# Optimization experiments

Measured on AMD Instinct MI355X. Metric: run time of the kernel, lower is better.

The kernel has to match this reference:

```python
import jax, jax.numpy as jnp
import numpy as np

H = 100  # hidden size

def setup_inputs() -> dict:
    key = jax.random.key(0)
    ks = jax.random.split(key, 7)
    B, T = 512, 1024
    s = 1.0 / np.sqrt(H)  # pytorch LSTMCell/Linear init scale
    return {
        "input": jax.random.normal(ks[0], (B, T), dtype=jnp.float32),
        "W_ih": jax.random.uniform(ks[1], (4 * H, 1), jnp.float32, -s, s),
        "W_hh": jax.random.uniform(ks[2], (4 * H, H), jnp.float32, -s, s),
        "b_ih": jax.random.uniform(ks[3], (4 * H,), jnp.float32, -s, s),
        "b_hh": jax.random.uniform(ks[4], (4 * H,), jnp.float32, -s, s),
        "W_out": jax.random.uniform(ks[5], (1, H), jnp.float32, -s, s),
        "b_out": jax.random.uniform(ks[6], (1,), jnp.float32, -s, s),
    }

def reference(input, W_ih, W_hh, b_ih, b_hh, W_out, b_out):
    B, T = input.shape
    dt = input.dtype
    # Precompute the input projection for all steps at once: [T, B, 4H]
    # (input_size == 1, so this is an outer product with W_ih[:, 0])
    x_proj = input.T[:, :, None] * W_ih[:, 0][None, None, :] + (b_ih + b_hh)

    def step(carry, xp_t):
        h, c = carry
        gates = xp_t + h @ W_hh.T  # [B, 4H]
        i, f, g, o = jnp.split(gates, 4, axis=1)  # PyTorch gate order i,f,g,o
        i = jax.nn.sigmoid(i)
        f = jax.nn.sigmoid(f)
        g = jnp.tanh(g)
        o = jax.nn.sigmoid(o)
        c_new = f * c + i * g
        h_new = o * jnp.tanh(c_new)
        out_t = h_new @ W_out.T + b_out  # [B, 1]
        return (h_new, c_new), out_t[:, 0]

    h0 = jnp.zeros((B, H), dtype=dt)
    c0 = jnp.zeros((B, H), dtype=dt)
    _, outs = jax.lax.scan(step, (h0, c0), x_proj)  # outs: [T, B]
    return outs.T  # [B, T]
```

## Files before the change

kernel.cpp:

```cpp
#include <hip/hip_runtime.h>


#define HID   100
#define TLEN  1024
#define NB    8
#define BLOCK 896
#define INSTR 1033
#define SC_LO 0.00048828125f
#define SC_HI 2048.0f

typedef _Float16 half8 __attribute__((ext_vector_type(8)));
typedef float    f32x4 __attribute__((ext_vector_type(4)));

#define MFMA(A,B,C) __builtin_amdgcn_mfma_f32_16x16x32_f16((A),(B),(C),0,0,0)
#define LOG2E   1.442695041f
#define LOG2E2  2.885390082f
#define RCP(x)  __builtin_amdgcn_rcpf(x)

static __device__ __forceinline__ unsigned packh(_Float16 a, _Float16 b) {
    return (unsigned)__builtin_bit_cast(unsigned short, a)
         | ((unsigned)__builtin_bit_cast(unsigned short, b) << 16);
}
static __device__ __forceinline__ float exp2v(float x) {
    float r;
    asm("v_exp_f32 %0, %1" : "=v"(r) : "v"(x));
    return r;
}

__global__ __launch_bounds__(BLOCK, 1)
void lstm_mfma5(
    const float* __restrict__ input,
    const float* __restrict__ W_ih,
    const float* __restrict__ W_hh,
    const float* __restrict__ b_ih,
    const float* __restrict__ b_hh,
    const float* __restrict__ W_out,
    const float* __restrict__ b_out,
    float* __restrict__ out)
{
    const int tid  = threadIdx.x;
    const int lane = tid & 63;
    const int w    = tid >> 6;
    const int b0   = blockIdx.x * NB;
    const int q    = lane >> 4;
    const int col  = lane & 15;
    const int side = (col >> 3) & 1;
    const int bat  = lane & 7;

    __shared__ __align__(16) unsigned B_lds[2][4][64][4];
    __shared__ float in_s[NB * INSTR];

    for (int i = tid; i < NB * TLEN; i += BLOCK) {
        const int n = i >> 10, t = i & 1023;
        in_s[n * INSTR + t] = input[(b0 + n) * TLEN + t];
    }
    for (int i = tid; i < 2 * 4 * 64 * 4; i += BLOCK)
        ((unsigned*)B_lds)[i] = 0u;

    const int nt = (w < 12) ? 2 : ((w == 12) ? 1 : 0);
    const int tb = 2 * w;

    half8 A[2][4];
    if (w < 13) {
        const int g = col & 3;
        const float scl = (g == 2) ? LOG2E2 : -LOG2E;
        #pragma unroll
        for (int i = 0; i < 2; ++i) {
            if (i < nt) {
                const int m    = tb + i;
                const int u    = 4 * m + (col >> 2);
                const int wrow = HID * g + u;
                #pragma unroll
                for (int kt = 0; kt < 4; ++kt) {
                    half8 hh;
                    #pragma unroll
                    for (int j = 0; j < 8; ++j) {
                        const int k = 32 * kt + 8 * q + j;
                        float v = 0.f;
                        if (k < HID)            v = W_hh[wrow * HID + k];
                        else if (k == HID)      v = b_ih[wrow] + b_hh[wrow];
                        else if (k <= HID + 2)  v = W_ih[wrow];
                        hh[j] = (_Float16)(v * scl);
                    }
                    A[i][kt] = hh;
                }
            }
        }
    } else {
        #pragma unroll
        for (int kt = 0; kt < 4; ++kt) {
            half8 hh;
            #pragma unroll
            for (int j = 0; j < 8; ++j) {
                const int k = 32 * kt + 8 * q + j;
                float v = 0.f;
                if (col == 0) {
                    if (k < HID)       v = W_out[k];
                    else if (k == HID) v = b_out[0];
                }
                hh[j] = (_Float16)v;
            }
            A[0][kt] = hh;
        }
    }

    float c0 = 0.f;

    __syncthreads();
    if (w == 13 && lane < NB) {
        const float xv = in_s[lane * INSTR];
        const _Float16 xh = (_Float16)xv;
        const _Float16 xl = (_Float16)(xv - (float)xh);
        uint2 dv; dv.x = packh((_Float16)1.f, xh); dv.y = packh(xl, (_Float16)0.f);
        *(uint2*)&B_lds[0][3][lane][2] = dv;
    }
    __syncthreads();

    #define CELLCORE(G0, G1, G2, G3, CC, UU) { \
        const float is_ = RCP(1.f + exp2v(G0)); \
        const float fs_ = RCP(1.f + exp2v(G1)); \
        const float os_ = RCP(1.f + exp2v(G3)); \
        const float gt_ = fmaf(-2.f, RCP(1.f + exp2v(G2)), 1.f); \
        CC = fmaf(fs_, CC, is_ * gt_); \
        const float th_ = fmaf(-2.f, RCP(1.f + exp2v(LOG2E2 * CC)), 1.f); \
        const float hf  = os_ * th_; \
        const _Float16 hh_ = (_Float16)hf; \
        const _Float16 hl_ = (_Float16)((hf - (float)hh_) * SC_HI); \
        unsigned short* hp0 = (unsigned short*)&B_lds[pp][(UU) >> 5] \
            [((((UU) >> 3) & 3) << 4) | bat][((UU) >> 1) & 3]; \
        hp0[(UU) & 1] = __builtin_bit_cast(unsigned short, hh_); \
        unsigned short* hp1 = (unsigned short*)&B_lds[pp][(UU) >> 5] \
            [((((UU) >> 3) & 3) << 4) | (bat + 8)][((UU) >> 1) & 3]; \
        hp1[(UU) & 1] = __builtin_bit_cast(unsigned short, hl_); \
    }

    #define CELLPAIR(DA, DB, UA, UB, CC) { \
        const float rA0 = __shfl_xor(DA[0], 8), rA1 = __shfl_xor(DA[1], 8); \
        const float rA2 = __shfl_xor(DA[2], 8), rA3 = __shfl_xor(DA[3], 8); \
        const float rB0 = __shfl_xor(DB[0], 8), rB1 = __shfl_xor(DB[1], 8); \
        const float rB2 = __shfl_xor(DB[2], 8), rB3 = __shfl_xor(DB[3], 8); \
        const float o0 = side ? DB[0] : DA[0], o1 = side ? DB[1] : DA[1]; \
        const float o2 = side ? DB[2] : DA[2], o3 = side ? DB[3] : DA[3]; \
        const float r0 = side ? rB0 : rA0, r1 = side ? rB1 : rA1; \
        const float r2 = side ? rB2 : rA2, r3 = side ? rB3 : rA3; \
        const float g0 = side ? fmaf(SC_LO, o0, r0) : fmaf(SC_LO, r0, o0); \
        const float g1 = side ? fmaf(SC_LO, o1, r1) : fmaf(SC_LO, r1, o1); \
        const float g2 = side ? fmaf(SC_LO, o2, r2) : fmaf(SC_LO, r2, o2); \
        const float g3 = side ? fmaf(SC_LO, o3, r3) : fmaf(SC_LO, r3, o3); \
        const int   uu = side ? (UB) : (UA); \
        CELLCORE(g0, g1, g2, g3, CC, uu) \
    }

    #define CELLLONE(DA, UA, CC) { \
        const float rA0 = __shfl_xor(DA[0], 8), rA1 = __shfl_xor(DA[1], 8); \
        const float rA2 = __shfl_xor(DA[2], 8), rA3 = __shfl_xor(DA[3], 8); \
        if (!side) { \
            const float g0 = fmaf(SC_LO, rA0, DA[0]); \
            const float g1 = fmaf(SC_LO, rA1, DA[1]); \
            const float g2 = fmaf(SC_LO, rA2, DA[2]); \
            const float g3 = fmaf(SC_LO, rA3, DA[3]); \
            CELLCORE(g0, g1, g2, g3, CC, (UA)) \
        } \
    }

    #pragma unroll 1
    for (int t = 0; t < TLEN; ++t) {
        const int p  = t & 1;
        const int pp = p ^ 1;
        const half8 bf0 = *(const half8*)&B_lds[p][0][lane][0];
        const half8 bf1 = *(const half8*)&B_lds[p][1][lane][0];
        const half8 bf2 = *(const half8*)&B_lds[p][2][lane][0];
        const half8 bf3 = *(const half8*)&B_lds[p][3][lane][0];

        if (w < 13) {
            f32x4 D0 = {0.f,0.f,0.f,0.f}, D1 = {0.f,0.f,0.f,0.f};
            D0 = MFMA(A[0][0], bf0, D0); D0 = MFMA(A[0][1], bf1, D0);
            D0 = MFMA(A[0][2], bf2, D0); D0 = MFMA(A[0][3], bf3, D0);
            if (nt == 2) {
                D1 = MFMA(A[1][0], bf0, D1); D1 = MFMA(A[1][1], bf1, D1);
                D1 = MFMA(A[1][2], bf2, D1); D1 = MFMA(A[1][3], bf3, D1);
                CELLPAIR(D0, D1, 4 * tb + q, 4 * (tb + 1) + q, c0)
            } else {
                CELLLONE(D0, 4 * tb + q, c0)
            }
        } else {
            f32x4 ao = {0.f,0.f,0.f,0.f};
            ao = MFMA(A[0][0], bf0, ao);
            ao = MFMA(A[0][1], bf1, ao);
            ao = MFMA(A[0][2], bf2, ao);
            ao = MFMA(A[0][3], bf3, ao);
            const float rv = __shfl_xor(ao[0], 8);
            if (lane < NB) {
                if (t > 0) out[(b0 + lane) * TLEN + (t - 1)] = fmaf(SC_LO, rv, ao[0]);
                if (t + 1 < TLEN) {
                    const float xv = in_s[lane * INSTR + (t + 1)];
                    const _Float16 xh = (_Float16)xv;
                    const _Float16 xl = (_Float16)(xv - (float)xh);
                    uint2 dv; dv.x = packh((_Float16)1.f, xh);
                    dv.y = packh(xl, (_Float16)0.f);
                    *(uint2*)&B_lds[pp][3][lane][2] = dv;
                }
            }
        }
        __syncthreads();
    }

    if (w == 13) {
        const half8 bf0 = *(const half8*)&B_lds[0][0][lane][0];
        const half8 bf1 = *(const half8*)&B_lds[0][1][lane][0];
        const half8 bf2 = *(const half8*)&B_lds[0][2][lane][0];
        const half8 bf3 = *(const half8*)&B_lds[0][3][lane][0];
        f32x4 ao = {0.f,0.f,0.f,0.f};
        ao = MFMA(A[0][0], bf0, ao);
        ao = MFMA(A[0][1], bf1, ao);
        ao = MFMA(A[0][2], bf2, ao);
        ao = MFMA(A[0][3], bf3, ao);
        const float rv = __shfl_xor(ao[0], 8);
        if (lane < NB) out[(b0 + lane) * TLEN + (TLEN - 1)] = fmaf(SC_LO, rv, ao[0]);
    }
}

extern "C" void kernel_launch(void* const* d_in, const int* in_sizes, int n_in,
                              void* d_out, int out_size, void* d_ws, size_t ws_size,
                              hipStream_t stream) {
    const float* input = (const float*)d_in[0];
    const float* W_ih  = (const float*)d_in[1];
    const float* W_hh  = (const float*)d_in[2];
    const float* b_ih  = (const float*)d_in[3];
    const float* b_hh  = (const float*)d_in[4];
    const float* W_out = (const float*)d_in[5];
    const float* b_out = (const float*)d_in[6];
    float* out = (float*)d_out;

    const int B = in_sizes[0] / TLEN;
    lstm_mfma5<<<B / NB, BLOCK, 0, stream>>>(input, W_ih, W_hh, b_ih, b_hh,
                                             W_out, b_out, out);
}
```

Baseline: 692.1 us.

## Drop compensated fp16 hi/lo split of hidden state and remap cell lanes

Stores the hidden state as a single fp16 value instead of a hi/lo residual pair, and removes the SC_LO recombination FMAs. This frees the second half of the MFMA B columns. Side-1 lanes now take the second tile's gates via one xor-8 shuffle, so every lane computes a useful cell instead of duplicating work. Wave 12 handles the leftover units alone, and LDS write addresses are precomputed once. The aim is to shorten the per-timestep serial critical path of shuffles, FMAs and LDS stores. The cost is lower precision in the recurrent matmul, which may drift over 1024 steps.

```diff
diff --git a/kernel.cpp b/kernel.cpp
--- a/kernel.cpp
+++ b/kernel.cpp
@@ -6,16 +6,14 @@
 #define NB    8
 #define BLOCK 896
 #define INSTR 1033
-#define SC_LO 0.00048828125f
-#define SC_HI 2048.0f
-
-typedef _Float16 half8 __attribute__((ext_vector_type(8)));
-typedef float    f32x4 __attribute__((ext_vector_type(4)));
-
-#define MFMA(A,B,C) __builtin_amdgcn_mfma_f32_16x16x32_f16((A),(B),(C),0,0,0)
 #define LOG2E   1.442695041f
 #define LOG2E2  2.885390082f
 #define RCP(x)  __builtin_amdgcn_rcpf(x)
+
+typedef _Float16 half8 __attribute__((ext_vector_type(8)));
+typedef float    f32x4 __attribute__((ext_vector_type(4)));
+
+#define MFMA(A,B,C) __builtin_amdgcn_mfma_f32_16x16x32_f16((A),(B),(C),0,0,0)
 
 static __device__ __forceinline__ unsigned packh(_Float16 a, _Float16 b) {
     return (unsigned)__builtin_bit_cast(unsigned short, a)
@@ -28,7 +26,7 @@
 }
 
 __global__ __launch_bounds__(BLOCK, 1)
-void lstm_mfma5(
+void lstm_mfma6(
     const float* __restrict__ input,
     const float* __restrict__ W_ih,
     const float* __restrict__ W_hh,
@@ -106,6 +104,13 @@
 
     float c0 = 0.f;
 
+    int my_u = 4 * tb + q + 4 * side;
+    if (w == 12) my_u = 96 + q;
+    char* const wbase = (char*)B_lds
+        + ((my_u >> 5) * 1024)
+        + (((((my_u >> 3) & 3) << 4) | bat) * 16)
+        + (((my_u >> 1) & 3) * 4) + ((my_u & 1) * 2);
+
     __syncthreads();
     if (w == 13 && lane < NB) {
         const float xv = in_s[lane * INSTR];
@@ -115,53 +120,6 @@
         *(uint2*)&B_lds[0][3][lane][2] = dv;
     }
     __syncthreads();
-
-    #define CELLCORE(G0, G1, G2, G3, CC, UU) { \
-        const float is_ = RCP(1.f + exp2v(G0)); \
-        const float fs_ = RCP(1.f + exp2v(G1)); \
-        const float os_ = RCP(1.f + exp2v(G3)); \
-        const float gt_ = fmaf(-2.f, RCP(1.f + exp2v(G2)), 1.f); \
-        CC = fmaf(fs_, CC, is_ * gt_); \
-        const float th_ = fmaf(-2.f, RCP(1.f + exp2v(LOG2E2 * CC)), 1.f); \
-        const float hf  = os_ * th_; \
-        const _Float16 hh_ = (_Float16)hf; \
-        const _Float16 hl_ = (_Float16)((hf - (float)hh_) * SC_HI); \
-        unsigned short* hp0 = (unsigned short*)&B_lds[pp][(UU) >> 5] \
-            [((((UU) >> 3) & 3) << 4) | bat][((UU) >> 1) & 3]; \
-        hp0[(UU) & 1] = __builtin_bit_cast(unsigned short, hh_); \
-        unsigned short* hp1 = (unsigned short*)&B_lds[pp][(UU) >> 5] \
-            [((((UU) >> 3) & 3) << 4) | (bat + 8)][((UU) >> 1) & 3]; \
-        hp1[(UU) & 1] = __builtin_bit_cast(unsigned short, hl_); \
-    }
-
-    #define CELLPAIR(DA, DB, UA, UB, CC) { \
-        const float rA0 = __shfl_xor(DA[0], 8), rA1 = __shfl_xor(DA[1], 8); \
-        const float rA2 = __shfl_xor(DA[2], 8), rA3 = __shfl_xor(DA[3], 8); \
-        const float rB0 = __shfl_xor(DB[0], 8), rB1 = __shfl_xor(DB[1], 8); \
-        const float rB2 = __shfl_xor(DB[2], 8), rB3 = __shfl_xor(DB[3], 8); \
-        const float o0 = side ? DB[0] : DA[0], o1 = side ? DB[1] : DA[1]; \
-        const float o2 = side ? DB[2] : DA[2], o3 = side ? DB[3] : DA[3]; \
-        const float r0 = side ? rB0 : rA0, r1 = side ? rB1 : rA1; \
-        const float r2 = side ? rB2 : rA2, r3 = side ? rB3 : rA3; \
-        const float g0 = side ? fmaf(SC_LO, o0, r0) : fmaf(SC_LO, r0, o0); \
-        const float g1 = side ? fmaf(SC_LO, o1, r1) : fmaf(SC_LO, r1, o1); \
-        const float g2 = side ? fmaf(SC_LO, o2, r2) : fmaf(SC_LO, r2, o2); \
-        const float g3 = side ? fmaf(SC_LO, o3, r3) : fmaf(SC_LO, r3, o3); \
-        const int   uu = side ? (UB) : (UA); \
-        CELLCORE(g0, g1, g2, g3, CC, uu) \
-    }
-
-    #define CELLLONE(DA, UA, CC) { \
-        const float rA0 = __shfl_xor(DA[0], 8), rA1 = __shfl_xor(DA[1], 8); \
-        const float rA2 = __shfl_xor(DA[2], 8), rA3 = __shfl_xor(DA[3], 8); \
-        if (!side) { \
-            const float g0 = fmaf(SC_LO, rA0, DA[0]); \
-            const float g1 = fmaf(SC_LO, rA1, DA[1]); \
-            const float g2 = fmaf(SC_LO, rA2, DA[2]); \
-            const float g3 = fmaf(SC_LO, rA3, DA[3]); \
-            CELLCORE(g0, g1, g2, g3, CC, (UA)) \
-        } \
-    }
 
     #pragma unroll 1
     for (int t = 0; t < TLEN; ++t) {
@@ -172,26 +130,53 @@
         const half8 bf2 = *(const half8*)&B_lds[p][2][lane][0];
         const half8 bf3 = *(const half8*)&B_lds[p][3][lane][0];
 
-        if (w < 13) {
+        if (w < 12) {
             f32x4 D0 = {0.f,0.f,0.f,0.f}, D1 = {0.f,0.f,0.f,0.f};
-            D0 = MFMA(A[0][0], bf0, D0); D0 = MFMA(A[0][1], bf1, D0);
-            D0 = MFMA(A[0][2], bf2, D0); D0 = MFMA(A[0][3], bf3, D0);
-            if (nt == 2) {
-                D1 = MFMA(A[1][0], bf0, D1); D1 = MFMA(A[1][1], bf1, D1);
-                D1 = MFMA(A[1][2], bf2, D1); D1 = MFMA(A[1][3], bf3, D1);
-                CELLPAIR(D0, D1, 4 * tb + q, 4 * (tb + 1) + q, c0)
-            } else {
-                CELLLONE(D0, 4 * tb + q, c0)
-            }
+            D0 = MFMA(A[0][0], bf0, D0); D1 = MFMA(A[1][0], bf0, D1);
+            D0 = MFMA(A[0][1], bf1, D0); D1 = MFMA(A[1][1], bf1, D1);
+            D0 = MFMA(A[0][2], bf2, D0); D1 = MFMA(A[1][2], bf2, D1);
+            D0 = MFMA(A[0][3], bf3, D0); D1 = MFMA(A[1][3], bf3, D1);
+            const float r0 = __shfl_xor(D1[0], 8);
+            const float r1 = __shfl_xor(D1[1], 8);
+            const float r2 = __shfl_xor(D1[2], 8);
+            const float r3 = __shfl_xor(D1[3], 8);
+            const float g0 = side ? r0 : D0[0];
+            const float g1 = side ? r1 : D0[1];
+            const float g2 = side ? r2 : D0[2];
+            const float g3 = side ? r3 : D0[3];
+            const float is_ = RCP(1.f + exp2v(g0));
+            const float fs_ = RCP(1.f + exp2v(g1));
+            const float os_ = RCP(1.f + exp2v(g3));
+            const float gt_ = fmaf(-2.f, RCP(1.f + exp2v(g2)), 1.f);
+            c0 = fmaf(fs_, c0, is_ * gt_);
+            const float th_ = fmaf(-2.f, RCP(1.f + exp2v(LOG2E2 * c0)), 1.f);
+            const _Float16 hh_ = (_Float16)(os_ * th_);
+            *(unsigned short*)(wbase + pp * 4096) =
+                __builtin_bit_cast(unsigned short, hh_);
+        } else if (w == 12) {
+            f32x4 D0 = {0.f,0.f,0.f,0.f};
+            D0 = MFMA(A[0][0], bf0, D0);
+            D0 = MFMA(A[0][1], bf1, D0);
+            D0 = MFMA(A[0][2], bf2, D0);
+            D0 = MFMA(A[0][3], bf3, D0);
+            const float is_ = RCP(1.f + exp2v(D0[0]));
+            const float fs_ = RCP(1.f + exp2v(D0[1]));
+            const float os_ = RCP(1.f + exp2v(D0[3]));
+            const float gt_ = fmaf(-2.f, RCP(1.f + exp2v(D0[2])), 1.f);
+            c0 = fmaf(fs_, c0, is_ * gt_);
+            const float th_ = fmaf(-2.f, RCP(1.f + exp2v(LOG2E2 * c0)), 1.f);
+            const _Float16 hh_ = (_Float16)(os_ * th_);
+            if (!side)
+                *(unsigned short*)(wbase + pp * 4096) =
+                    __builtin_bit_cast(unsigned short, hh_);
         } else {
             f32x4 ao = {0.f,0.f,0.f,0.f};
             ao = MFMA(A[0][0], bf0, ao);
             ao = MFMA(A[0][1], bf1, ao);
             ao = MFMA(A[0][2], bf2, ao);
             ao = MFMA(A[0][3], bf3, ao);
-            const float rv = __shfl_xor(ao[0], 8);
             if (lane < NB) {
-                if (t > 0) out[(b0 + lane) * TLEN + (t - 1)] = fmaf(SC_LO, rv, ao[0]);
+                if (t > 0) out[(b0 + lane) * TLEN + (t - 1)] = ao[0];
                 if (t + 1 < TLEN) {
                     const float xv = in_s[lane * INSTR + (t + 1)];
                     const _Float16 xh = (_Float16)xv;
@@ -215,8 +200,7 @@
         ao = MFMA(A[0][1], bf1, ao);
         ao = MFMA(A[0][2], bf2, ao);
         ao = MFMA(A[0][3], bf3, ao);
-        const float rv = __shfl_xor(ao[0], 8);
-        if (lane < NB) out[(b0 + lane) * TLEN + (TLEN - 1)] = fmaf(SC_LO, rv, ao[0]);
+        if (lane < NB) out[(b0 + lane) * TLEN + (TLEN - 1)] = ao[0];
     }
 }
 
@@ -233,6 +217,6 @@
     float* out = (float*)d_out;
 
     const int B = in_sizes[0] / TLEN;
-    lstm_mfma5<<<B / NB, BLOCK, 0, stream>>>(input, W_ih, W_hh, b_ih, b_hh,
+    lstm_mfma6<<<B / NB, BLOCK, 0, stream>>>(input, W_ih, W_hh, b_ih, b_hh,
                                              W_out, b_out, out);
 }
```

After: 574.0 us. 17.1% less time.
